# Kernel optimization log

Hardware: AMD Instinct MI355X
Metric: run time of the kernel (lower is better)

Reference implementation:

```python
import jax, jax.numpy as jnp
import numpy as np

N_NODES = 200000
BATCH = 400000
EMB = 64

def setup_inputs() -> dict:
    key = jax.random.key(0)
    k1, k2, k3, k4, k5 = jax.random.split(key, 5)
    return {
        "actions_idx": jax.random.randint(k1, (BATCH,), 0, N_NODES),
        "node_embedding": jax.random.normal(k2, (N_NODES, EMB), dtype=jnp.float32),
        "state_embedding": jax.random.normal(k3, (BATCH, EMB), dtype=jnp.float32),
        "W_4": jax.random.normal(k4, (EMB, 1), dtype=jnp.float32),
        "W_5": jax.random.normal(k5, (EMB, 1), dtype=jnp.float32),
    }

def reference(actions_idx, node_embedding, state_embedding, W_4, W_5):
    # Z_a = sparse.mm(actions, node_embedding) with one-hot action rows == gather
    Z_a = node_embedding[actions_idx]                     # [B, E]
    # (Z_a outer Z_s) @ W_4 == Z_a * (Z_s @ W_4): avoid the [B,E,E] intermediate
    s = state_embedding @ W_4                             # [B, 1]
    Q_s_a = jax.nn.relu(Z_a * s) @ W_5                    # [B, 1]
    return Q_s_a
```

## Files before the change

kernel.cpp:

```cpp
#include <hip/hip_runtime.h>


typedef float f4 __attribute__((ext_vector_type(4)));

__global__ __launch_bounds__(256) void Decoding_43404939493634_kernel(
    const int*   __restrict__ idx,
    const float* __restrict__ node,
    const float* __restrict__ state,
    const float* __restrict__ W4,
    const float* __restrict__ W5,
    float*       __restrict__ out,
    int B)
{
    const int lane16 = threadIdx.x & 15;

    const f4 w4 = reinterpret_cast<const f4*>(W4)[lane16];
    const f4 w5 = reinterpret_cast<const f4*>(W5)[lane16];

    const int group   = (blockIdx.x * blockDim.x + threadIdx.x) >> 4;
    const int ngroups = (gridDim.x * blockDim.x) >> 4;

    int a_next = (group < B) ? __builtin_nontemporal_load(idx + group) : 0;

    for (int row = group; row < B; row += ngroups) {
        const int a = a_next;
        const int nrow = row + ngroups;
        if (nrow < B) a_next = __builtin_nontemporal_load(idx + nrow);

        const f4 se = __builtin_nontemporal_load(
            reinterpret_cast<const f4*>(state + (size_t)row * 64) + lane16);
        const f4 ne = reinterpret_cast<const f4*>(node + (size_t)a * 64)[lane16];

        float s = se.x * w4.x + se.y * w4.y + se.z * w4.z + se.w * w4.w;
        #pragma unroll
        for (int o = 1; o < 16; o <<= 1) s += __shfl_xor(s, o);

        float q = fmaxf(ne.x * s, 0.f) * w5.x
                + fmaxf(ne.y * s, 0.f) * w5.y
                + fmaxf(ne.z * s, 0.f) * w5.z
                + fmaxf(ne.w * s, 0.f) * w5.w;
        #pragma unroll
        for (int o = 1; o < 16; o <<= 1) q += __shfl_xor(q, o);

        if (lane16 == 0)
            __builtin_nontemporal_store(q, out + row);
    }
}

extern "C" void kernel_launch(void* const* d_in, const int* in_sizes, int n_in,
                              void* d_out, int out_size, void* d_ws, size_t ws_size,
                              hipStream_t stream) {
    const int*   idx   = (const int*)  d_in[0];
    const float* node  = (const float*)d_in[1];
    const float* state = (const float*)d_in[2];
    const float* W4    = (const float*)d_in[3];
    const float* W5    = (const float*)d_in[4];
    float*       out   = (float*)d_out;

    const int B = in_sizes[0];

    const int block  = 256;
    const int blocks = 2048;
    Decoding_43404939493634_kernel<<<blocks, block, 0, stream>>>(
        idx, node, state, W4, W5, out, B);
}
```

Before: 37.12 us.

## Precompute per-node positive/negative ReLU projections and gather compact pairs

The code uses relu(x*s) = s*relu(x) when s>=0 and -s*relu(-x) otherwise, so each node's W5 dot products with relu(ne) and relu(-ne) are computed once into a float2 table in workspace. The main kernel then gathers 8 bytes per row instead of a 256-byte node row, which swaps a large random-access read for one sequential pass over the node table. It adds a second launch and depends on enough workspace, otherwise it falls back to a fused kernel. The persistent grid-stride loop and nontemporal hints are also dropped in favour of one row per 16-lane group.

```diff
diff --git a/kernel.cpp b/kernel.cpp
--- a/kernel.cpp
+++ b/kernel.cpp
@@ -3,7 +3,59 @@
 
 typedef float f4 __attribute__((ext_vector_type(4)));
 
-__global__ __launch_bounds__(256) void Decoding_43404939493634_kernel(
+__global__ __launch_bounds__(256) void Decoding_precompute_AB(
+    const float* __restrict__ node,
+    const float* __restrict__ W5,
+    float2*      __restrict__ AB,
+    int N)
+{
+    const int lane16 = threadIdx.x & 15;
+    const int n = (int)((blockIdx.x * blockDim.x + threadIdx.x) >> 4);
+    if (n >= N) return;
+
+    const f4 w5 = reinterpret_cast<const f4*>(W5)[lane16];
+    const f4 ne = reinterpret_cast<const f4*>(node + (size_t)n * 64)[lane16];
+
+    float a = fmaxf(ne.x, 0.f) * w5.x + fmaxf(ne.y, 0.f) * w5.y
+            + fmaxf(ne.z, 0.f) * w5.z + fmaxf(ne.w, 0.f) * w5.w;
+    float b = fmaxf(-ne.x, 0.f) * w5.x + fmaxf(-ne.y, 0.f) * w5.y
+            + fmaxf(-ne.z, 0.f) * w5.z + fmaxf(-ne.w, 0.f) * w5.w;
+
+    #pragma unroll
+    for (int o = 1; o < 16; o <<= 1) {
+        a += __shfl_xor(a, o);
+        b += __shfl_xor(b, o);
+    }
+    if (lane16 == 0) AB[n] = make_float2(a, b);
+}
+
+__global__ __launch_bounds__(256) void Decoding_main(
+    const int*    __restrict__ idx,
+    const float*  __restrict__ state,
+    const float*  __restrict__ W4,
+    const float2* __restrict__ AB,
+    float*        __restrict__ out,
+    int B)
+{
+    const int lane16 = threadIdx.x & 15;
+    const int row = (int)((blockIdx.x * blockDim.x + threadIdx.x) >> 4);
+    if (row >= B) return;
+
+    const f4 w4 = reinterpret_cast<const f4*>(W4)[lane16];
+
+    const int a = idx[row];
+    const float2 ab = AB[a];
+    const f4 se = reinterpret_cast<const f4*>(state + (size_t)row * 64)[lane16];
+
+    float s = se.x * w4.x + se.y * w4.y + se.z * w4.z + se.w * w4.w;
+    #pragma unroll
+    for (int o = 1; o < 16; o <<= 1) s += __shfl_xor(s, o);
+
+    if (lane16 == 0)
+        out[row] = (s >= 0.f) ? s * ab.x : (-s) * ab.y;
+}
+
+__global__ __launch_bounds__(256) void Decoding_fused_fallback(
     const int*   __restrict__ idx,
     const float* __restrict__ node,
     const float* __restrict__ state,
@@ -13,38 +65,29 @@
     int B)
 {
     const int lane16 = threadIdx.x & 15;
+    const int row = (int)((blockIdx.x * blockDim.x + threadIdx.x) >> 4);
+    if (row >= B) return;
 
     const f4 w4 = reinterpret_cast<const f4*>(W4)[lane16];
     const f4 w5 = reinterpret_cast<const f4*>(W5)[lane16];
 
-    const int group   = (blockIdx.x * blockDim.x + threadIdx.x) >> 4;
-    const int ngroups = (gridDim.x * blockDim.x) >> 4;
+    const int a = idx[row];
+    const f4 se = reinterpret_cast<const f4*>(state + (size_t)row * 64)[lane16];
+    const f4 ne = reinterpret_cast<const f4*>(node + (size_t)a * 64)[lane16];
 
-    int a_next = (group < B) ? __builtin_nontemporal_load(idx + group) : 0;
-
-    for (int row = group; row < B; row += ngroups) {
-        const int a = a_next;
-        const int nrow = row + ngroups;
-        if (nrow < B) a_next = __builtin_nontemporal_load(idx + nrow);
-
-        const f4 se = __builtin_nontemporal_load(
-            reinterpret_cast<const f4*>(state + (size_t)row * 64) + lane16);
-        const f4 ne = reinterpret_cast<const f4*>(node + (size_t)a * 64)[lane16];
-
-        float s = se.x * w4.x + se.y * w4.y + se.z * w4.z + se.w * w4.w;
-        #pragma unroll
-        for (int o = 1; o < 16; o <<= 1) s += __shfl_xor(s, o);
-
-        float q = fmaxf(ne.x * s, 0.f) * w5.x
-                + fmaxf(ne.y * s, 0.f) * w5.y
-                + fmaxf(ne.z * s, 0.f) * w5.z
-                + fmaxf(ne.w * s, 0.f) * w5.w;
-        #pragma unroll
-        for (int o = 1; o < 16; o <<= 1) q += __shfl_xor(q, o);
-
-        if (lane16 == 0)
-            __builtin_nontemporal_store(q, out + row);
+    float s = se.x * w4.x + se.y * w4.y + se.z * w4.z + se.w * w4.w;
+    float pa = fmaxf(ne.x, 0.f) * w5.x + fmaxf(ne.y, 0.f) * w5.y
+             + fmaxf(ne.z, 0.f) * w5.z + fmaxf(ne.w, 0.f) * w5.w;
+    float pb = fmaxf(-ne.x, 0.f) * w5.x + fmaxf(-ne.y, 0.f) * w5.y
+             + fmaxf(-ne.z, 0.f) * w5.z + fmaxf(-ne.w, 0.f) * w5.w;
+    #pragma unroll
+    for (int o = 1; o < 16; o <<= 1) {
+        s += __shfl_xor(s, o);
+        pa += __shfl_xor(pa, o);
+        pb += __shfl_xor(pb, o);
     }
+    if (lane16 == 0)
+        out[row] = (s >= 0.f) ? s * pa : (-s) * pb;
 }
 
 extern "C" void kernel_launch(void* const* d_in, const int* in_sizes, int n_in,
@@ -58,9 +101,17 @@
     float*       out   = (float*)d_out;
 
     const int B = in_sizes[0];
+    const int N = in_sizes[1] / 64;
 
-    const int block  = 256;
-    const int blocks = 2048;
-    Decoding_43404939493634_kernel<<<blocks, block, 0, stream>>>(
-        idx, node, state, W4, W5, out, B);
+    if (ws_size >= (size_t)N * sizeof(float2)) {
+        float2* AB = (float2*)d_ws;
+        const int blk1 = (N + 15) / 16;
+        Decoding_precompute_AB<<<blk1, 256, 0, stream>>>(node, W5, AB, N);
+        const int blk2 = (B + 15) / 16;
+        Decoding_main<<<blk2, 256, 0, stream>>>(idx, state, W4, AB, out, B);
+    } else {
+        const int blk = (B + 15) / 16;
+        Decoding_fused_fallback<<<blk, 256, 0, stream>>>(
+            idx, node, state, W4, W5, out, B);
+    }
 }
```

After: 38.41 us. +3.5%, slower.
